# Optimization experiments

Hardware: AMD Instinct MI355X
Metric: run time of the kernel (lower is better)

## Reference

```python
import jax, jax.numpy as jnp
import numpy as np

B, N, DIM, H, DH, PDIM, ED = 2, 384, 256, 4, 64, 128, 16
EPS = 1e-8


def _ln(x, g, b):
    m = x.mean(-1, keepdims=True)
    v = ((x - m) ** 2).mean(-1, keepdims=True)
    return (x - m) / jnp.sqrt(v + 1e-5) * g + b


def setup_inputs() -> dict:
    key = jax.random.key(0)
    ks = iter(jax.random.split(key, 48))
    def rn(shape, s=0.02):
        return jax.random.normal(next(ks), shape, jnp.float32) * s
    z = lambda *s: jnp.zeros(s, jnp.float32)
    o = lambda *s: jnp.ones(s, jnp.float32)
    return dict(
        feats=jax.random.normal(next(ks), (B, N, DIM), jnp.float32),
        coors=jax.random.normal(next(ks), (B, N, 3), jnp.float32),
        edges=jax.random.normal(next(ks), (B, N, N, ED), jnp.float32),
        gamma=o(DIM),
        w_qkv=rn((DIM, 3 * H * DH)),
        w_gate=z(DIM, 2 * H), b_gate=jnp.full((2 * H,), 10.0, jnp.float32),
        w_th=rn((H, H), 0.3),
        w_e1=rn((H + ED, 2 * (H + ED))), w_e2=rn((2 * (H + ED), H)),
        w_c=rn((H, H)),
        w_cg=rn((H, H)), b_cg=z(H),
        coors_scale=o(1),
        coors_combine=jax.random.normal(next(ks), (H,), jnp.float32),
        pb_w0=rn((1, PDIM)), pb_b0=z(PDIM), pb_g0=o(PDIM), pb_be0=z(PDIM),
        pb_w1=rn((PDIM, PDIM)), pb_b1=z(PDIM), pb_g1=o(PDIM), pb_be1=z(PDIM),
        pb_w2=rn((PDIM, PDIM)), pb_b2=z(PDIM), pb_g2=o(PDIM), pb_be2=z(PDIM),
        w_qkpos=rn((PDIM, H)), b_qkpos=z(H),
        w_vpos=rn((PDIM, H * DH)), b_vpos=z(H * DH),
        w_out=rn((H * DH, DIM)), b_out=z(DIM),
    )


def reference(feats, coors, edges, gamma, w_qkv, w_gate, b_gate, w_th, w_e1, w_e2,
              w_c, w_cg, b_cg, coors_scale, coors_combine,
              pb_w0, pb_b0, pb_g0, pb_be0, pb_w1, pb_b1, pb_g1, pb_be1,
              pb_w2, pb_b2, pb_g2, pb_be2, w_qkpos, b_qkpos, w_vpos, b_vpos,
              w_out, b_out):
    b, n, _ = feats.shape
    h, dh = H, DH
    x = _ln(feats, gamma, 0.0)                                  # pre-norm (beta is a zero buffer)
    rel_coors = coors[:, :, None, :] - coors[:, None, :, :]      # b i j 3
    rel_dist = jnp.linalg.norm(rel_coors, axis=-1)               # b i j

    qkv = x @ w_qkv
    q, k, v = jnp.split(qkv, 3, axis=-1)
    q = q.reshape(b, n, h, dh).transpose(0, 2, 1, 3)             # b h n d
    k = k.reshape(b, n, h, dh).transpose(0, 2, 1, 3)
    v = v.reshape(b, n, h, dh).transpose(0, 2, 1, 3)

    gates = jax.nn.sigmoid(x @ w_gate + b_gate).reshape(b, n, 2, h)
    out_gate = gates[:, :, 0].transpose(0, 2, 1)[..., None]      # b h n 1
    rel_out_gate = gates[:, :, 1].transpose(0, 2, 1)[..., None]  # b h n 1

    # dynamic position bias MLP on pairwise distances (input_dim=1)
    p = rel_dist[..., None]                                      # b i j 1
    p = jax.nn.silu(_ln(p @ pb_w0 + pb_b0, pb_g0, pb_be0))
    p = jax.nn.silu(_ln(p @ pb_w1 + pb_b1, pb_g1, pb_be1))
    p = jax.nn.silu(_ln(p @ pb_w2 + pb_b2, pb_g2, pb_be2))       # b i j pdim
    qk_pos = (p @ w_qkpos + b_qkpos).transpose(0, 3, 1, 2)       # b h i j
    value_pos = (p @ w_vpos + b_vpos).reshape(b, n, n, h, dh).transpose(0, 3, 1, 2, 4)  # b h i j d

    q = q * (dh ** -0.5)
    qk = jnp.einsum('bhid,bhjd->bhij', q, k) + qk_pos            # b h i j

    # edge MLP fused with per-head scores
    qk_e = jnp.concatenate([qk.transpose(0, 2, 3, 1), edges], axis=-1)  # b i j (h+ed)
    cmi = jax.nn.gelu(qk_e @ w_e1, approximate=False) @ w_e2     # b i j h
    qk = cmi.transpose(0, 3, 1, 2)                               # b h i j

    # coordinate attention branch (edge variant: GELU -> Linear(h,h))
    coor_weights = jax.nn.gelu(cmi, approximate=False) @ w_c     # b i j h
    coor_attn = jax.nn.softmax(coor_weights, axis=-2)            # softmax over j
    rel_sign = cmi @ w_cg + b_cg                                 # b i j h

    nrm = jnp.linalg.norm(rel_coors, axis=-1, keepdims=True)
    rel_norm = rel_coors / jnp.maximum(nrm, EPS) * coors_scale   # CoorsNorm, b i j 3

    attn = jax.nn.softmax(qk, axis=-1)
    attn = jnp.einsum('hg,bgij->bhij', w_th, attn)               # talking heads 1x1 conv

    node_out = jnp.einsum('bhij,bhjd->bhid', attn, v) \
             + jnp.einsum('bhij,bhijd->bhid', attn, value_pos)   # b h i d

    w = coor_attn * rel_sign                                     # b i j h
    coors_out = jnp.einsum('bijh,bijc->bhic', w, rel_norm)       # b h i 3

    node_out = node_out * out_gate
    coors_out = coors_out * rel_out_gate
    coors_out = jnp.einsum('bhic,h->bic', coors_out, coors_combine)
    node_out = node_out.transpose(0, 2, 1, 3).reshape(b, n, h * dh)
    return node_out @ w_out + b_out, coors_out
```

## Files before the change

### kernel.cpp

```cpp
#include <hip/hip_runtime.h>
#include <hip/hip_bf16.h>

#define B_   2
#define N_   384
#define DIM_ 256
#define H_   4
#define DH_  64
#define PD_  128
#define ED_  16
#define NT_  24
#define TPB_ 300
#define JOBS_ 600

typedef _Float16 v8h __attribute__((ext_vector_type(8)));
typedef float    v4f __attribute__((ext_vector_type(4)));

__device__ __forceinline__ float rcp_(float x) { return __builtin_amdgcn_rcpf(x); }

__device__ __forceinline__ float erf_fast(float x) {
    float ax = fabsf(x);
    float t = rcp_(fmaf(0.3275911f, ax, 1.0f));
    float y = t * fmaf(t, fmaf(t, fmaf(t, fmaf(t, 1.061405429f, -1.453152027f),
                                       1.421413741f), -0.284496736f), 0.254829592f);
    float r = 1.0f - y * __expf(-ax * ax);
    return (x < 0.f) ? -r : r;
}
__device__ __forceinline__ float gelu_(float x) {
    return 0.5f * x * (1.0f + erf_fast(x * 0.70710678118654752f));
}
__device__ __forceinline__ float silu_(float x) {
    return x * rcp_(1.0f + __expf(-x));
}

__device__ __forceinline__ float2 block_reduce256_f2(float2 v, float2* red) {
    #pragma unroll
    for (int o = 32; o > 0; o >>= 1) {
        v.x += __shfl_xor(v.x, o); v.y += __shfl_xor(v.y, o);
    }
    __syncthreads();
    if ((threadIdx.x & 63) == 0) red[threadIdx.x >> 6] = v;
    __syncthreads();
    float2 r = red[0];
    #pragma unroll
    for (int w2 = 1; w2 < 4; w2++) {
        float2 o = red[w2];
        r.x += o.x; r.y += o.y;
    }
    return r;
}

__device__ __forceinline__ void block_reduce8(float4& va, float4& vb, bool ismax,
                                              float4* red, int base) {
    #pragma unroll
    for (int o = 32; o > 0; o >>= 1) {
        float ax = __shfl_xor(va.x, o), ay = __shfl_xor(va.y, o);
        float az = __shfl_xor(va.z, o), aw = __shfl_xor(va.w, o);
        float bx = __shfl_xor(vb.x, o), by = __shfl_xor(vb.y, o);
        float bz = __shfl_xor(vb.z, o), bw = __shfl_xor(vb.w, o);
        if (ismax) {
            va.x = fmaxf(va.x, ax); va.y = fmaxf(va.y, ay); va.z = fmaxf(va.z, az); va.w = fmaxf(va.w, aw);
            vb.x = fmaxf(vb.x, bx); vb.y = fmaxf(vb.y, by); vb.z = fmaxf(vb.z, bz); vb.w = fmaxf(vb.w, bw);
        } else {
            va.x += ax; va.y += ay; va.z += az; va.w += aw;
            vb.x += bx; vb.y += by; vb.z += bz; vb.w += bw;
        }
    }
    if ((threadIdx.x & 63) == 0) {
        red[base * 8 + (threadIdx.x >> 6)]       = va;
        red[(base + 1) * 8 + (threadIdx.x >> 6)] = vb;
    }
    __syncthreads();
    va = red[base * 8]; vb = red[(base + 1) * 8];
    #pragma unroll
    for (int w2 = 1; w2 < 6; w2++) {
        float4 oa = red[base * 8 + w2], ob = red[(base + 1) * 8 + w2];
        if (ismax) {
            va.x = fmaxf(va.x, oa.x); va.y = fmaxf(va.y, oa.y); va.z = fmaxf(va.z, oa.z); va.w = fmaxf(va.w, oa.w);
            vb.x = fmaxf(vb.x, ob.x); vb.y = fmaxf(vb.y, ob.y); vb.z = fmaxf(vb.z, ob.z); vb.w = fmaxf(vb.w, ob.w);
        } else {
            va.x += oa.x; va.y += oa.y; va.z += oa.z; va.w += oa.w;
            vb.x += ob.x; vb.y += ob.y; vb.z += ob.z; vb.w += ob.w;
        }
    }
}

__global__ __launch_bounds__(256) void eq_k1(
    const float* __restrict__ feats, const float* __restrict__ gamma,
    const float* __restrict__ w_qkv, const float* __restrict__ w_gate,
    const float* __restrict__ b_gate,
    _Float16* __restrict__ qh, _Float16* __restrict__ kh, float* __restrict__ v,
    float* __restrict__ og, float* __restrict__ rg) {
    const int r0 = blockIdx.x * 2;
    const int b = r0 / N_;
    const int t = threadIdx.x;
    __shared__ float xs[2][DIM_];
    __shared__ float2 red2k[4];
    __shared__ float gredS[16][17];
    float2 f;
    f.x = feats[(long)(r0 + 0) * DIM_ + t];
    f.y = feats[(long)(r0 + 1) * DIM_ + t];
    float2 s = block_reduce256_f2(f, red2k);
    float mx = s.x * (1.f/DIM_), my = s.y * (1.f/DIM_);
    float2 d = make_float2(f.x - mx, f.y - my);
    float2 vr = block_reduce256_f2(make_float2(d.x*d.x, d.y*d.y), red2k);
    float g = gamma[t];
    xs[0][t] = d.x * rsqrtf(vr.x * (1.f/DIM_) + 1e-5f) * g;
    xs[1][t] = d.y * rsqrtf(vr.y * (1.f/DIM_) + 1e-5f) * g;
    __syncthreads();
    float acc[6];
    #pragma unroll
    for (int k = 0; k < 6; k++) acc[k] = 0.f;
    for (int c = 0; c < DIM_; c++) {
        const float* wr = w_qkv + (long)c * 768;
        float w0 = wr[t], w1 = wr[t + 256], w2 = wr[t + 512];
        #pragma unroll
        for (int r = 0; r < 2; r++) {
            float xc = xs[r][c];
            acc[r * 3 + 0] += xc * w0;
            acc[r * 3 + 1] += xc * w1;
            acc[r * 3 + 2] += xc * w2;
        }
    }
    int h = t >> 6, dd = t & 63;
    #pragma unroll
    for (int r = 0; r < 2; r++) {
        int n = r0 + r - b * N_;
        long idx = ((long)(b * H_ + h) * N_ + n) * DH_ + dd;
        qh[idx] = (_Float16)(acc[r * 3 + 0] * 0.125f);
        kh[idx] = (_Float16)(acc[r * 3 + 1]);
        v[idx]  = acc[r * 3 + 2];
    }
    {
        const int o = t & 15, chunk = t >> 4;
        const int gg = o & 7, rr = o >> 3;
        float part = 0.f;
        #pragma unroll
        for (int k = 0; k < 16; k++) {
            int c = chunk * 16 + k;
            part += xs[rr][c] * w_gate[c * 8 + gg];
        }
        gredS[chunk][o] = part;
    }
    __syncthreads();
    if (t < 16) {
        float a = b_gate[t & 7];
        #pragma unroll
        for (int k = 0; k < 16; k++) a += gredS[k][t];
        float gv = rcp_(1.0f + __expf(-a));
        int rr2 = t >> 3, g2 = t & 7;
        int n = r0 + rr2 - b * N_;
        if (g2 < 4) og[(b * H_ + g2) * N_ + n] = gv;
        else        rg[(b * H_ + (g2 - 4)) * N_ + n] = gv;
    }
}

#define MFMA16(a, b, c) __builtin_amdgcn_mfma_f32_16x16x32_f16(a, b, c, 0, 0, 0)

#define LNAPPLY(gr_, ber_)                                                        \
{                                                                                  \
    _Pragma("unroll")                                                              \
    for (int rg2 = 0; rg2 < 4; rg2++) {                                            \
        float s = 0.f, sq = 0.f;                                                   \
        _Pragma("unroll")                                                          \
        for (int nt = 0; nt < 8; nt++) {                                           \
            float v0 = acc[nt][rg2]; s += v0; sq += v0 * v0;                       \
        }                                                                          \
        s += __shfl_xor(s, 1); sq += __shfl_xor(sq, 1);                            \
        s += __shfl_xor(s, 2); sq += __shfl_xor(sq, 2);                            \
        s += __shfl_xor(s, 4); sq += __shfl_xor(sq, 4);                            \
        s += __shfl_xor(s, 8); sq += __shfl_xor(sq, 8);                            \
        float mean = s * (1.f / 128.f);                                            \
        float inv = rsqrtf(sq * (1.f / 128.f) - mean * mean + 1e-5f);              \
        int row2 = quad * 4 + rg2;                                                 \
        _Pragma("unroll")                                                          \
        for (int nt = 0; nt < 8; nt++) {                                           \
            float y = (acc[nt][rg2] - mean) * inv * gr_[nt] + ber_[nt];            \
            myslice[row2 * 136 + nt * 16 + l15] = (_Float16)silu_(y);              \
        }                                                                          \
    }                                                                              \
}

__global__ __launch_bounds__(512) __attribute__((amdgpu_waves_per_eu(2, 2)))
void eq_k2(
    const float* __restrict__ coors,
    const float* __restrict__ w0, const float* __restrict__ b0,
    const float* __restrict__ g0, const float* __restrict__ be0,
    const float* __restrict__ W1g, const float* __restrict__ b1,
    const float* __restrict__ g1, const float* __restrict__ be1,
    const float* __restrict__ W2g, const float* __restrict__ b2,
    const float* __restrict__ g2, const float* __restrict__ be2,
    const float* __restrict__ wqk, const float* __restrict__ bqk,
    const _Float16* __restrict__ qh, const _Float16* __restrict__ kh,
    _Float16* __restrict__ pT, float* __restrict__ qkpos,
    float* __restrict__ qkq) {

    extern __shared__ char smem[];
    _Float16* W1T    = (_Float16*)smem;
    _Float16* W2T    = (_Float16*)(smem + 34816);
    _Float16* wqT    = (_Float16*)(smem + 69632);
    float*    PQR    = (float*)(smem + 73984);
    _Float16* slices = (_Float16*)(smem + 75520);

    const int t = threadIdx.x;
    const int lane = t & 63, wv = t >> 6;
    const int l15 = lane & 15, quad = lane >> 4;

    for (int idx = t; idx < 16384; idx += 512) {
        int k = idx >> 7, n = idx & 127;
        W1T[n * 136 + k] = (_Float16)W1g[idx];
        W2T[n * 136 + k] = (_Float16)W2g[idx];
    }
    for (int idx = t; idx < 2048; idx += 512) {
        int n = idx >> 7, k = idx & 127;
        wqT[n * 136 + k] = (n < 4) ? (_Float16)wqk[k * 4 + n] : (_Float16)0.f;
    }
    float Sw = 0, Sb = 0, Sww = 0, Swb = 0, Sbb = 0;
    for (int c = 0; c < 128; c++) {
        float w = w0[c], bb2v = b0[c];
        Sw += w; Sb += bb2v; Sww += w * w; Swb += w * bb2v; Sbb += bb2v * bb2v;
    }
    const float mw = Sw * (1.f / 128.f), mbb = Sb * (1.f / 128.f);
    const float A2 = Sww * (1.f / 128.f) - mw * mw;
    const float AD = Swb * (1.f / 128.f) - mw * mbb;
    const float D2 = Sbb * (1.f / 128.f) - mbb * mbb;
    if (t < 128) {
        PQR[t]       = (w0[t] - mw) * g0[t];
        PQR[128 + t] = (b0[t] - mbb) * g0[t];
        PQR[256 + t] = be0[t];
    }
    float b1r[8], b2r[8], g1r[8], be1r[8], g2r[8], be2r[8];
    #pragma unroll
    for (int nt = 0; nt < 8; nt++) {
        int c = nt * 16 + l15;
        b1r[nt] = b1[c]; b2r[nt] = b2[c];
        g1r[nt] = g1[c]; be1r[nt] = be1[c];
        g2r[nt] = g2[c]; be2r[nt] = be2[c];
    }
    const float bqv = (l15 < 4) ? bqk[l15] : 0.f;
    __syncthreads();

    for (int jo = blockIdx.x; jo < JOBS_; jo += 256) {
        int b = jo / TPB_;
        int tt2 = jo - b * TPB_;
        int it = 0, rl = NT_;
        while (tt2 >= rl) { tt2 -= rl; it++; rl--; }
        const int jt = it + tt2;
        const int j0 = jt * 16;

        #pragma unroll 1
        for (int rr = 0; rr < 2; rr++) {
            const int r = wv + rr * 8;
            const int ii = it * 16 + r;
            _Float16* myslice = slices + r * 2176;
            const float cix = coors[(b * N_ + ii) * 3 + 0];
            const float ciy = coors[(b * N_ + ii) * 3 + 1];
            const float ciz = coors[(b * N_ + ii) * 3 + 2];
            float tt, uu;
            {
                int j = j0 + l15;
                float dx = cix - coors[(b * N_ + j) * 3 + 0];
                float dy = ciy - coors[(b * N_ + j) * 3 + 1];
                float dz = ciz - coors[(b * N_ + j) * 3 + 2];
                float d = sqrtf(dx * dx + dy * dy + dz * dz);
                float var = (d * d) * A2 + 2.f * d * AD + D2;
                float inv = rsqrtf(var + 1e-5f);
                tt = d * inv; uu = inv;
            }
            v8h A[4];
            #pragma unroll
            for (int kt = 0; kt < 4; kt++) {
                int base = kt * 32 + quad * 8;
                float4 Pa = *(const float4*)&PQR[base],       Pb = *(const float4*)&PQR[base + 4];
                float4 Qa = *(const float4*)&PQR[128 + base], Qb = *(const float4*)&PQR[128 + base + 4];
                float4 Ra = *(const float4*)&PQR[256 + base], Rb = *(const float4*)&PQR[256 + base + 4];
                float Pj[8] = {Pa.x, Pa.y, Pa.z, Pa.w, Pb.x, Pb.y, Pb.z, Pb.w};
                float Qj[8] = {Qa.x, Qa.y, Qa.z, Qa.w, Qb.x, Qb.y, Qb.z, Qb.w};
                float Rj[8] = {Ra.x, Ra.y, Ra.z, Ra.w, Rb.x, Rb.y, Rb.z, Rb.w};
                v8h av;
                #pragma unroll
                for (int jj = 0; jj < 8; jj++) {
                    float y = tt * Pj[jj] + uu * Qj[jj] + Rj[jj];
                    av[jj] = (_Float16)silu_(y);
                }
                A[kt] = av;
            }
            v4f acc[8];
            #pragma unroll
            for (int nt = 0; nt < 8; nt++) {
                v4f ci = {b1r[nt], b1r[nt], b1r[nt], b1r[nt]};
                acc[nt] = ci;
            }
            #pragma unroll
            for (int kt = 0; kt < 4; kt++) {
                #pragma unroll
                for (int nt = 0; nt < 8; nt++) {
                    v8h Bv = *(const v8h*)&W1T[(nt * 16 + l15) * 136 + kt * 32 + quad * 8];
                    acc[nt] = MFMA16(A[kt], Bv, acc[nt]);
                }
            }
            LNAPPLY(g1r, be1r)
            #pragma unroll
            for (int kt = 0; kt < 4; kt++)
                A[kt] = *(const v8h*)&myslice[l15 * 136 + kt * 32 + quad * 8];
            #pragma unroll
            for (int nt = 0; nt < 8; nt++) {
                v4f ci = {b2r[nt], b2r[nt], b2r[nt], b2r[nt]};
                acc[nt] = ci;
            }
            #pragma unroll
            for (int kt = 0; kt < 4; kt++) {
                #pragma unroll
                for (int nt = 0; nt < 8; nt++) {
                    v8h Bv = *(const v8h*)&W2T[(nt * 16 + l15) * 136 + kt * 32 + quad * 8];
                    acc[nt] = MFMA16(A[kt], Bv, acc[nt]);
                }
            }
            LNAPPLY(g2r, be2r)
            {
                v4f c = {0.f, 0.f, 0.f, 0.f};
                #pragma unroll
                for (int kt = 0; kt < 4; kt++) {
                    v8h av = *(const v8h*)&myslice[l15 * 136 + kt * 32 + quad * 8];
                    v8h wq = *(const v8h*)&wqT[l15 * 136 + kt * 32 + quad * 8];
                    c = MFMA16(av, wq, c);
                }
                if (l15 < 4) {
                    #pragma unroll
                    for (int rg2 = 0; rg2 < 4; rg2++) {
                        int rowj = quad * 4 + rg2;
                        float val = c[rg2] + bqv;
                        qkpos[((long)(b * N_ + ii) * N_ + j0 + rowj) * 4 + l15] = val;
                        if (it != jt)
                            qkpos[((long)(b * N_ + j0 + rowj) * N_ + ii) * 4 + l15] = val;
                    }
                }
            }
        }
        __syncthreads();

        #pragma unroll
        for (int rx = 0; rx < 2; rx++) {
            const int r2 = wv * 2 + rx;
            {
                const _Float16* src = slices + r2 * 2176;
                _Float16* chunk = pT + (((long)(b * N_ + it * 16 + r2) * 24 + jt) << 11);
                #pragma unroll
                for (int cc = 0; cc < 2; cc++) {
                    int c = lane + cc * 64;
                    v8h lo, hi;
                    #pragma unroll
                    for (int k = 0; k < 8; k++) {
                        lo[k] = src[k * 136 + c];
                        hi[k] = src[(k + 8) * 136 + c];
                    }
                    *(v8h*)(chunk + c * 16)     = lo;
                    *(v8h*)(chunk + c * 16 + 8) = hi;
                }
            }
            if (it != jt) {
                _Float16* chunk = pT + (((long)(b * N_ + jt * 16 + r2) * 24 + it) << 11);
                #pragma unroll
                for (int cc = 0; cc < 2; cc++) {
                    int c = lane + cc * 64;
                    v8h lo, hi;
                    #pragma unroll
                    for (int r = 0; r < 8; r++) {
                        lo[r] = slices[r * 2176 + r2 * 136 + c];
                        hi[r] = slices[(r + 8) * 2176 + r2 * 136 + c];
                    }
                    *(v8h*)(chunk + c * 16)     = lo;
                    *(v8h*)(chunk + c * 16 + 8) = hi;
                }
            }
        }
        __syncthreads();
    }

    {
        int gw = (blockIdx.x - 88) * 8 + wv;
        if (blockIdx.x >= 88 && gw < 384) {
            const int bh = gw / 48;
            const int rest = gw - bh * 48;
            const int it = rest >> 1, nh = rest & 1;
            const int bb = bh >> 2, hh = bh & 3;
            const int i0 = it * 16;
            v8h A0 = *(const v8h*)&qh[((long)(bh * N_) + i0 + l15) * DH_ + quad * 8];
            v8h A1 = *(const v8h*)&qh[((long)(bh * N_) + i0 + l15) * DH_ + 32 + quad * 8];
            #pragma unroll 1
            for (int nt = 0; nt < 12; nt++) {
                int jq0 = nh * 192 + nt * 16;
                v8h B0 = *(const v8h*)&kh[((long)(bh * N_) + jq0 + l15) * DH_ + quad * 8];
                v8h B1 = *(const v8h*)&kh[((long)(bh * N_) + jq0 + l15) * DH_ + 32 + quad * 8];
                v4f c = {0.f, 0.f, 0.f, 0.f};
                c = MFMA16(A0, B0, c);
                c = MFMA16(A1, B1, c);
                #pragma unroll
                for (int rg2 = 0; rg2 < 4; rg2++) {
                    int i = i0 + quad * 4 + rg2;
                    int j = jq0 + l15;
                    long idx = (((long)(bb * N_ + i)) * N_ + j) * 4 + hh;
                    qkq[idx] = c[rg2];
                }
            }
        }
    }
}

__global__ __launch_bounds__(256) void eq_k3a(
    const float* __restrict__ edges, const float* __restrict__ qkpos,
    float* __restrict__ qkq,
    const float* __restrict__ w_e1, const float* __restrict__ w_e2) {
    __shared__ _Float16 we1h[20 * 40];
    __shared__ float we2[40 * 4];
    const int t = threadIdx.x;
    for (int idx = t; idx < 800; idx += 256) we1h[idx] = (_Float16)w_e1[idx];
    if (t < 160) we2[t] = w_e2[t];
    __syncthreads();

    const long pair = (long)blockIdx.x * 256 + t;
    float in20[20];
    {
        float4 qp = *(const float4*)(qkpos + pair * 4);
        float4 qq = *(const float4*)(qkq + pair * 4);
        in20[0] = qp.x + qq.x; in20[1] = qp.y + qq.y;
        in20[2] = qp.z + qq.z; in20[3] = qp.w + qq.w;
    }
    const float4* ep = (const float4*)(edges + pair * ED_);
    float4 e0 = ep[0], e1 = ep[1], e2 = ep[2], e3 = ep[3];
    in20[4] = e0.x;  in20[5] = e0.y;  in20[6] = e0.z;  in20[7] = e0.w;
    in20[8] = e1.x;  in20[9] = e1.y;  in20[10] = e1.z; in20[11] = e1.w;
    in20[12] = e2.x; in20[13] = e2.y; in20[14] = e2.z; in20[15] = e2.w;
    in20[16] = e3.x; in20[17] = e3.y; in20[18] = e3.z; in20[19] = e3.w;

    float c0 = 0, c1 = 0, c2 = 0, c3 = 0;
    #pragma unroll 1
    for (int oc = 0; oc < 5; oc++) {
        float a8[8] = {0.f, 0.f, 0.f, 0.f, 0.f, 0.f, 0.f, 0.f};
        #pragma unroll
        for (int c = 0; c < 20; c++) {
            float xc = in20[c];
            v8h wv = *(const v8h*)&we1h[c * 40 + oc * 8];
            #pragma unroll
            for (int o2 = 0; o2 < 8; o2++) a8[o2] += xc * (float)wv[o2];
        }
        #pragma unroll
        for (int o = 0; o < 8; o++) {
            float gg = gelu_(a8[o]);
            float4 w2v = *(const float4*)&we2[(oc * 8 + o) * 4];
            c0 += gg * w2v.x; c1 += gg * w2v.y; c2 += gg * w2v.z; c3 += gg * w2v.w;
        }
    }
    *(float4*)(qkq + pair * 4) = make_float4(c0, c1, c2, c3);
}

__global__ __launch_bounds__(384) void eq_k3b(
    const float* __restrict__ cmig,
    const _Float16* __restrict__ pT, const float* __restrict__ v,
    const float* __restrict__ coors,
    const float* __restrict__ w_c, const float* __restrict__ w_cg,
    const float* __restrict__ b_cg, const float* __restrict__ w_th,
    const float* __restrict__ cscale, const float* __restrict__ ccomb,
    const float* __restrict__ og, const float* __restrict__ rg,
    const float* __restrict__ w_vpos, const float* __restrict__ b_vpos,
    const float* __restrict__ w_out, const float* __restrict__ b_out,
    float* __restrict__ out0, float* __restrict__ out1) {
    int row = blockIdx.x;
    int b = row / N_, i = row - b * N_;
    int j = threadIdx.x;
    __shared__ float wcs[16], wcgs[16], bcgs[4], wths[16];
    __shared__ float attnS[4 * N_];
    __shared__ float apS[2 * 4 * PD_];
    __shared__ float nodeS[256];
    __shared__ float4 red4[50];

    if (j < 16) { wcs[j] = w_c[j]; wcgs[j] = w_cg[j]; wths[j] = w_th[j]; }
    if (j < 4) bcgs[j] = b_cg[j];
    __syncthreads();

    long pair = ((long)row) * N_ + j;
    float4 cm = *(const float4*)(cmig + pair * 4);
    float cmi[4] = {cm.x, cm.y, cm.z, cm.w};
    float gc[4], cp[4], rs[4];
    #pragma unroll
    for (int h = 0; h < 4; h++) gc[h] = gelu_(cmi[h]);
    #pragma unroll
    for (int h = 0; h < 4; h++) {
        cp[h] = gc[0] * wcs[h] + gc[1] * wcs[4 + h] + gc[2] * wcs[8 + h] + gc[3] * wcs[12 + h];
        rs[h] = cmi[0] * wcgs[h] + cmi[1] * wcgs[4 + h] + cmi[2] * wcgs[8 + h] + cmi[3] * wcgs[12 + h] + bcgs[h];
    }

    float dx = coors[(b * N_ + i) * 3 + 0] - coors[(b * N_ + j) * 3 + 0];
    float dy = coors[(b * N_ + i) * 3 + 1] - coors[(b * N_ + j) * 3 + 1];
    float dz = coors[(b * N_ + i) * 3 + 2] - coors[(b * N_ + j) * 3 + 2];
    float nrm = sqrtf(dx * dx + dy * dy + dz * dz);
    float sc = cscale[0] * rcp_(fmaxf(nrm, 1e-8f));
    float rx = dx * sc, ry = dy * sc, rz = dz * sc;

    float4 m4  = make_float4(cmi[0], cmi[1], cmi[2], cmi[3]);
    float4 cm4 = make_float4(cp[0], cp[1], cp[2], cp[3]);
    block_reduce8(m4, cm4, true, red4, 0);
    float e[4], ec[4];
    e[0] = __expf(cmi[0] - m4.x); e[1] = __expf(cmi[1] - m4.y);
    e[2] = __expf(cmi[2] - m4.z); e[3] = __expf(cmi[3] - m4.w);
    ec[0] = __expf(cp[0] - cm4.x); ec[1] = __expf(cp[1] - cm4.y);
    ec[2] = __expf(cp[2] - cm4.z); ec[3] = __expf(cp[3] - cm4.w);
    float4 l4  = make_float4(e[0], e[1], e[2], e[3]);
    float4 cl4 = make_float4(ec[0], ec[1], ec[2], ec[3]);
    block_reduce8(l4, cl4, false, red4, 2);

    float sm[4] = {e[0] * rcp_(l4.x), e[1] * rcp_(l4.y), e[2] * rcp_(l4.z), e[3] * rcp_(l4.w)};
    #pragma unroll
    for (int h = 0; h < 4; h++)
        attnS[h * N_ + j] = wths[h * 4 + 0] * sm[0] + wths[h * 4 + 1] * sm[1]
                          + wths[h * 4 + 2] * sm[2] + wths[h * 4 + 3] * sm[3];

    float w[4] = {ec[0] * rcp_(cl4.x) * rs[0], ec[1] * rcp_(cl4.y) * rs[1],
                  ec[2] * rcp_(cl4.z) * rs[2], ec[3] * rcp_(cl4.w) * rs[3]};
    float rv[12];
    #pragma unroll
    for (int h = 0; h < 4; h++) { rv[h] = w[h] * rx; rv[4 + h] = w[h] * ry; rv[8 + h] = w[h] * rz; }
    #pragma unroll
    for (int o = 32; o > 0; o >>= 1) {
        #pragma unroll
        for (int k = 0; k < 12; k++) rv[k] += __shfl_xor(rv[k], o);
    }
    if ((j & 63) == 0) {
        int wid = j >> 6;
        red4[32 + wid * 3 + 0] = make_float4(rv[0], rv[1], rv[2], rv[3]);
        red4[32 + wid * 3 + 1] = make_float4(rv[4], rv[5], rv[6], rv[7]);
        red4[32 + wid * 3 + 2] = make_float4(rv[8], rv[9], rv[10], rv[11]);
    }
    __syncthreads();
    if (j == 0) {
        float4 sx4 = red4[32], sy4 = red4[33], sz4 = red4[34];
        #pragma unroll
        for (int w2 = 1; w2 < 6; w2++) {
            float4 ax = red4[32 + w2 * 3 + 0], ay = red4[32 + w2 * 3 + 1], az = red4[32 + w2 * 3 + 2];
            sx4.x += ax.x; sx4.y += ax.y; sx4.z += ax.z; sx4.w += ax.w;
            sy4.x += ay.x; sy4.y += ay.y; sy4.z += ay.z; sy4.w += ay.w;
            sz4.x += az.x; sz4.y += az.y; sz4.z += az.z; sz4.w += az.w;
        }
        float f0 = ccomb[0] * rg[(b * H_ + 0) * N_ + i];
        float f1 = ccomb[1] * rg[(b * H_ + 1) * N_ + i];
        float f2 = ccomb[2] * rg[(b * H_ + 2) * N_ + i];
        float f3 = ccomb[3] * rg[(b * H_ + 3) * N_ + i];
        out1[(b * N_ + i) * 3 + 0] = f0 * sx4.x + f1 * sx4.y + f2 * sx4.z + f3 * sx4.w;
        out1[(b * N_ + i) * 3 + 1] = f0 * sy4.x + f1 * sy4.y + f2 * sy4.z + f3 * sy4.w;
        out1[(b * N_ + i) * 3 + 2] = f0 * sz4.x + f1 * sz4.y + f2 * sz4.z + f3 * sz4.w;
    }

    if (j < 128) {
        const int lane = j & 63, l15d = lane & 15, quadd = lane >> 4;
        const int parity = j >> 6;
        const int hh = l15d & 3;
        const float msk = (l15d < 4) ? 1.f : 0.f;
        v4f acc[8];
        #pragma unroll
        for (int nt = 0; nt < 8; nt++) { v4f z = {0.f, 0.f, 0.f, 0.f}; acc[nt] = z; }
        #pragma unroll 2
        for (int kth = 0; kth < 6; kth++) {
            int kt = parity * 6 + kth;
            float4 a0 = *(const float4*)&attnS[hh * N_ + kt * 32 + quadd * 8];
            float4 a1 = *(const float4*)&attnS[hh * N_ + kt * 32 + quadd * 8 + 4];
            v8h Af;
            Af[0] = (_Float16)(a0.x * msk); Af[1] = (_Float16)(a0.y * msk);
            Af[2] = (_Float16)(a0.z * msk); Af[3] = (_Float16)(a0.w * msk);
            Af[4] = (_Float16)(a1.x * msk); Af[5] = (_Float16)(a1.y * msk);
            Af[6] = (_Float16)(a1.z * msk); Af[7] = (_Float16)(a1.w * msk);
            const _Float16* chunkp = pT + (((long)row * 24 + kt * 2 + (quadd >> 1)) << 11)
                                        + ((quadd & 1) << 3);
            #pragma unroll
            for (int nt = 0; nt < 8; nt++) {
                v8h Bv = *(const v8h*)&chunkp[(nt * 16 + l15d) * 16];
                acc[nt] = MFMA16(Af, Bv, acc[nt]);
            }
        }
        if (quadd == 0) {
            #pragma unroll
            for (int nt = 0; nt < 8; nt++)
                #pragma unroll
                for (int rg2 = 0; rg2 < 4; rg2++)
                    apS[parity * 512 + rg2 * 128 + nt * 16 + l15d] = acc[nt][rg2];
        }
    } else {
        int tt = j - 128, h = tt >> 6, d = tt & 63;
        float acc0 = 0, acc1 = 0, acc2 = 0, acc3 = 0;
        const float* vp = v + ((long)(b * H_ + h) * N_) * DH_ + d;
        #pragma unroll 8
        for (int jj = 0; jj < N_; jj += 4) {
            float4 a = *(const float4*)&attnS[h * N_ + jj];
            acc0 += a.x * vp[(long)(jj + 0) * DH_];
            acc1 += a.y * vp[(long)(jj + 1) * DH_];
            acc2 += a.z * vp[(long)(jj + 2) * DH_];
            acc3 += a.w * vp[(long)(jj + 3) * DH_];
        }
        nodeS[tt] = (acc0 + acc1) + (acc2 + acc3);
    }
    __syncthreads();

    if (j < 256) {
        int h = j >> 6, d = j & 63;
        float accp = 0;
        const float* wv = w_vpos + h * DH_ + d;
        #pragma unroll 4
        for (int c4 = 0; c4 < 32; c4++) {
            float4 p0 = *(const float4*)&apS[h * 128 + c4 * 4];
            float4 p1 = *(const float4*)&apS[512 + h * 128 + c4 * 4];
            accp += (p0.x + p1.x) * wv[(long)(c4 * 4 + 0) * (H_ * DH_)]
                  + (p0.y + p1.y) * wv[(long)(c4 * 4 + 1) * (H_ * DH_)]
                  + (p0.z + p1.z) * wv[(long)(c4 * 4 + 2) * (H_ * DH_)]
                  + (p0.w + p1.w) * wv[(long)(c4 * 4 + 3) * (H_ * DH_)];
        }
        float Sh = wths[h * 4 + 0] + wths[h * 4 + 1] + wths[h * 4 + 2] + wths[h * 4 + 3];
        nodeS[j] = (nodeS[j] + accp + Sh * b_vpos[h * DH_ + d]) * og[(b * H_ + h) * N_ + i];
    }
    __syncthreads();

    if (j < 256) {
        float acc = b_out[j];
        const float* wo = w_out + j;
        #pragma unroll 4
        for (int c4 = 0; c4 < 64; c4++) {
            float4 nv4 = *(const float4*)&nodeS[c4 * 4];
            acc += nv4.x * wo[(long)(c4 * 4 + 0) * 256]
                 + nv4.y * wo[(long)(c4 * 4 + 1) * 256]
                 + nv4.z * wo[(long)(c4 * 4 + 2) * 256]
                 + nv4.w * wo[(long)(c4 * 4 + 3) * 256];
        }
        out0[(long)row * 256 + j] = acc;
    }
}

extern "C" void kernel_launch(void* const* d_in, const int* in_sizes, int n_in,
                              void* d_out, int out_size, void* d_ws, size_t ws_size,
                              hipStream_t stream) {
    (void)in_sizes; (void)n_in; (void)out_size; (void)ws_size;
    const float* feats   = (const float*)d_in[0];
    const float* coors   = (const float*)d_in[1];
    const float* edges   = (const float*)d_in[2];
    const float* gamma   = (const float*)d_in[3];
    const float* w_qkv   = (const float*)d_in[4];
    const float* w_gate  = (const float*)d_in[5];
    const float* b_gate  = (const float*)d_in[6];
    const float* w_th    = (const float*)d_in[7];
    const float* w_e1    = (const float*)d_in[8];
    const float* w_e2    = (const float*)d_in[9];
    const float* w_c     = (const float*)d_in[10];
    const float* w_cg    = (const float*)d_in[11];
    const float* b_cg    = (const float*)d_in[12];
    const float* cscale  = (const float*)d_in[13];
    const float* ccomb   = (const float*)d_in[14];
    const float* pb_w0   = (const float*)d_in[15];
    const float* pb_b0   = (const float*)d_in[16];
    const float* pb_g0   = (const float*)d_in[17];
    const float* pb_be0  = (const float*)d_in[18];
    const float* pb_w1   = (const float*)d_in[19];
    const float* pb_b1   = (const float*)d_in[20];
    const float* pb_g1   = (const float*)d_in[21];
    const float* pb_be1  = (const float*)d_in[22];
    const float* pb_w2   = (const float*)d_in[23];
    const float* pb_b2   = (const float*)d_in[24];
    const float* pb_g2   = (const float*)d_in[25];
    const float* pb_be2  = (const float*)d_in[26];
    const float* w_qkpos = (const float*)d_in[27];
    const float* b_qkpos = (const float*)d_in[28];
    const float* w_vpos  = (const float*)d_in[29];
    const float* b_vpos  = (const float*)d_in[30];
    const float* w_out   = (const float*)d_in[31];
    const float* b_out   = (const float*)d_in[32];

    char* ws = (char*)d_ws;
    _Float16* qh   = (_Float16*)(ws + 0);
    _Float16* kh   = (_Float16*)(ws + 393216);
    float* v       = (float*)(ws + 786432);
    float* og      = (float*)(ws + 1572864);
    float* rg      = (float*)(ws + 1585152);
    float* qkpos   = (float*)(ws + 1597440);
    _Float16* pT   = (_Float16*)(ws + 6316032);
    float* qkq     = (float*)(ws + 81813504);

    float* out0 = (float*)d_out;
    float* out1 = out0 + (long)B_ * N_ * DIM_;

    const int K2_LDS = 145152;
    hipFuncSetAttribute((const void*)eq_k2, hipFuncAttributeMaxDynamicSharedMemorySize, K2_LDS);

    eq_k1<<<384, 256, 0, stream>>>(feats, gamma, w_qkv, w_gate, b_gate, qh, kh, v, og, rg);
    eq_k2<<<256, 512, K2_LDS, stream>>>(coors, pb_w0, pb_b0, pb_g0, pb_be0,
                                        pb_w1, pb_b1, pb_g1, pb_be1,
                                        pb_w2, pb_b2, pb_g2, pb_be2,
                                        w_qkpos, b_qkpos, qh, kh, pT, qkpos, qkq);
    eq_k3a<<<(B_ * N_ * N_) / 256, 256, 0, stream>>>(edges, qkpos, qkq, w_e1, w_e2);
    eq_k3b<<<B_ * N_, 384, 0, stream>>>(qkq, pT, v, coors,
                                        w_c, w_cg, b_cg, w_th,
                                        cscale, ccomb, og, rg,
                                        w_vpos, b_vpos, w_out, b_out, out0, out1);
}
```

Baseline: 280.2 us.

## Split pairwise-bias tile jobs into half-tiles to balance blocks and cut LDS

Measured after the change: 271.6 us. 3.1% less time.

```diff
diff --git a/kernel.cpp b/kernel.cpp
--- a/kernel.cpp
+++ b/kernel.cpp
@@ -10,7 +10,7 @@
 #define ED_  16
 #define NT_  24
 #define TPB_ 300
-#define JOBS_ 600
+#define HJOBS_ 1200
 
 typedef _Float16 v8h __attribute__((ext_vector_type(8)));
 typedef float    v4f __attribute__((ext_vector_type(4)));
@@ -239,19 +239,19 @@
     const float bqv = (l15 < 4) ? bqk[l15] : 0.f;
     __syncthreads();
 
-    for (int jo = blockIdx.x; jo < JOBS_; jo += 256) {
-        int b = jo / TPB_;
-        int tt2 = jo - b * TPB_;
+    for (int jo = blockIdx.x; jo < HJOBS_; jo += 256) {
+        const int tile = jo >> 1, half = jo & 1;
+        int b = tile / TPB_;
+        int tt2 = tile - b * TPB_;
         int it = 0, rl = NT_;
         while (tt2 >= rl) { tt2 -= rl; it++; rl--; }
         const int jt = it + tt2;
         const int j0 = jt * 16;
 
-        #pragma unroll 1
-        for (int rr = 0; rr < 2; rr++) {
-            const int r = wv + rr * 8;
-            const int ii = it * 16 + r;
-            _Float16* myslice = slices + r * 2176;
+        const int r = half * 8 + wv;
+        const int ii = it * 16 + r;
+        _Float16* myslice = slices + wv * 2176;
+        {
             const float cix = coors[(b * N_ + ii) * 3 + 0];
             const float ciy = coors[(b * N_ + ii) * 3 + 1];
             const float ciz = coors[(b * N_ + ii) * 3 + 2];
@@ -336,40 +336,37 @@
                 }
             }
         }
+
+        {
+            _Float16* chunk = pT + (((long)(b * N_ + ii) * 24 + jt) << 11);
+            #pragma unroll
+            for (int cc = 0; cc < 2; cc++) {
+                int c = lane + cc * 64;
+                v8h lo, hi;
+                #pragma unroll
+                for (int k = 0; k < 8; k++) {
+                    lo[k] = myslice[k * 136 + c];
+                    hi[k] = myslice[(k + 8) * 136 + c];
+                }
+                *(v8h*)(chunk + c * 16)     = lo;
+                *(v8h*)(chunk + c * 16 + 8) = hi;
+            }
+        }
         __syncthreads();
 
-        #pragma unroll
-        for (int rx = 0; rx < 2; rx++) {
-            const int r2 = wv * 2 + rx;
-            {
-                const _Float16* src = slices + r2 * 2176;
-                _Float16* chunk = pT + (((long)(b * N_ + it * 16 + r2) * 24 + jt) << 11);
+        if (it != jt) {
+            #pragma unroll
+            for (int rx = 0; rx < 2; rx++) {
+                const int r2 = wv * 2 + rx;
+                _Float16* chunk = pT + (((long)(b * N_ + jt * 16 + r2) * 24 + it) << 11);
                 #pragma unroll
                 for (int cc = 0; cc < 2; cc++) {
                     int c = lane + cc * 64;
-                    v8h lo, hi;
+                    v8h m;
                     #pragma unroll
-                    for (int k = 0; k < 8; k++) {
-                        lo[k] = src[k * 136 + c];
-                        hi[k] = src[(k + 8) * 136 + c];
-                    }
-                    *(v8h*)(chunk + c * 16)     = lo;
-                    *(v8h*)(chunk + c * 16 + 8) = hi;
-                }
-            }
-            if (it != jt) {
-                _Float16* chunk = pT + (((long)(b * N_ + jt * 16 + r2) * 24 + it) << 11);
-                #pragma unroll
-                for (int cc = 0; cc < 2; cc++) {
-                    int c = lane + cc * 64;
-                    v8h lo, hi;
-                    #pragma unroll
-                    for (int r = 0; r < 8; r++) {
-                        lo[r] = slices[r * 2176 + r2 * 136 + c];
-                        hi[r] = slices[(r + 8) * 2176 + r2 * 136 + c];
-                    }
-                    *(v8h*)(chunk + c * 16)     = lo;
-                    *(v8h*)(chunk + c * 16 + 8) = hi;
+                    for (int k = 0; k < 8; k++)
+                        m[k] = slices[k * 2176 + r2 * 136 + c];
+                    *(v8h*)(chunk + c * 16 + half * 8) = m;
                 }
             }
         }
@@ -377,8 +374,8 @@
     }
 
     {
-        int gw = (blockIdx.x - 88) * 8 + wv;
-        if (blockIdx.x >= 88 && gw < 384) {
+        int gw = (blockIdx.x - 176) * 8 + wv;
+        if (blockIdx.x >= 176 && blockIdx.x < 224 && gw < 384) {
             const int bh = gw / 48;
             const int rest = gw - bh * 48;
             const int it = rest >> 1, nh = rest & 1;
@@ -682,7 +679,7 @@
     float* out0 = (float*)d_out;
     float* out1 = out0 + (long)B_ * N_ * DIM_;
 
-    const int K2_LDS = 145152;
+    const int K2_LDS = 110336;
     hipFuncSetAttribute((const void*)eq_k2, hipFuncAttributeMaxDynamicSharedMemorySize, K2_LDS);
 
     eq_k1<<<384, 256, 0, stream>>>(feats, gamma, w_qkv, w_gate, b_gate, qh, kh, v, og, rg);
```
